# Kernel optimization log

Measured on AMD Instinct MI355X. Metric: run time of the kernel, lower is better.

The kernel has to match this reference:

```python
import jax, jax.numpy as jnp
import numpy as np

# init config (matches init_kwargs)
NO_TRANS = False
SPATIAL_SCALE = 0.0625
POOLED = 7
SAMPLES = 2          # sampling_ratio (sample_per_part)
TRANS_STD = 0.1

B, C, H, W = 2, 256, 96, 96
N_ROIS = 512


def setup_inputs() -> dict:
    key = jax.random.key(0)
    k1, k2, k3, k4, k5 = jax.random.split(key, 5)
    bottom_data = jax.random.normal(k1, (B, C, H, W), dtype=jnp.float32)
    img = H / SPATIAL_SCALE  # image-space extent (1536)
    bidx = jax.random.randint(k2, (N_ROIS,), 0, B).astype(jnp.float32)
    xy1 = jax.random.uniform(k3, (N_ROIS, 2), minval=0.0, maxval=0.7 * img)
    wh = jax.random.uniform(k4, (N_ROIS, 2), minval=0.05 * img, maxval=0.3 * img)
    bottom_rois = jnp.concatenate([bidx[:, None], xy1, xy1 + wh], axis=1)  # [N,5]
    bottom_trans = jax.random.normal(k5, (N_ROIS, 2, POOLED, POOLED), dtype=jnp.float32)
    return {"bottom_data": bottom_data, "bottom_rois": bottom_rois, "bottom_trans": bottom_trans}


def _deform_psroi_pool(feat, rois, trans):
    # feat [B,C,H,W], rois [N,5], trans [N,2,P,P] -> out [N,C,P,P]
    Hf, Wf = feat.shape[2], feat.shape[3]
    b = rois[:, 0].astype(jnp.int32)                                    # [N]
    # CUDA kernel rounds roi coords, shifts by -0.5
    x1 = jnp.round(rois[:, 1]) * SPATIAL_SCALE - 0.5
    y1 = jnp.round(rois[:, 2]) * SPATIAL_SCALE - 0.5
    x2 = (jnp.round(rois[:, 3]) + 1.0) * SPATIAL_SCALE - 0.5
    y2 = (jnp.round(rois[:, 4]) + 1.0) * SPATIAL_SCALE - 0.5
    rw = jnp.maximum(x2 - x1, 0.1)
    rh = jnp.maximum(y2 - y1, 0.1)
    bin_w = rw / POOLED
    bin_h = rh / POOLED
    sub_w = bin_w / SAMPLES
    sub_h = bin_h / SAMPLES

    grid = jnp.arange(POOLED, dtype=feat.dtype)
    # part_size == pooled_size and group_size == 1 -> part_h=ph, part_w=pw, class 0
    if NO_TRANS:
        trans_x = jnp.zeros((rois.shape[0], POOLED, POOLED), feat.dtype)
        trans_y = trans_x
    else:
        trans_x = trans[:, 0] * TRANS_STD  # [N,P,P]
        trans_y = trans[:, 1] * TRANS_STD

    # bin start coords per (n, ph, pw)
    wstart = grid[None, None, :] * bin_w[:, None, None] + x1[:, None, None] + trans_x * rw[:, None, None]
    hstart = grid[None, :, None] * bin_h[:, None, None] + y1[:, None, None] + trans_y * rh[:, None, None]

    s = jnp.arange(SAMPLES, dtype=feat.dtype)
    # sample coords [N,P,P,S(ih),S(iw)]
    w = wstart[:, :, :, None, None] + s[None, None, None, None, :] * sub_w[:, None, None, None, None]
    h = hstart[:, :, :, None, None] + s[None, None, None, :, None] * sub_h[:, None, None, None, None]

    valid = (w >= -0.5) & (w <= Wf - 0.5) & (h >= -0.5) & (h <= Hf - 0.5)
    wc = jnp.clip(w, 0.0, Wf - 1.0)
    hc = jnp.clip(h, 0.0, Hf - 1.0)
    x0 = jnp.floor(wc); y0 = jnp.floor(hc)
    dx = wc - x0; dy = hc - y0
    x0i = x0.astype(jnp.int32); y0i = y0.astype(jnp.int32)
    x1i = jnp.ceil(wc).astype(jnp.int32); y1i = jnp.ceil(hc).astype(jnp.int32)

    feat_hwc = jnp.transpose(feat, (0, 2, 3, 1))  # [B,H,W,C]
    bb = b[:, None, None, None, None]

    def gather(yi, xi):
        return feat_hwc[bb, yi, xi]  # [N,P,P,S,S,C]

    w00 = ((1.0 - dx) * (1.0 - dy))[..., None]
    w01 = (dx * (1.0 - dy))[..., None]
    w10 = ((1.0 - dx) * dy)[..., None]
    w11 = (dx * dy)[..., None]
    val = (w00 * gather(y0i, x0i) + w01 * gather(y0i, x1i)
           + w10 * gather(y1i, x0i) + w11 * gather(y1i, x1i))
    val = jnp.where(valid[..., None], val, 0.0)

    ssum = val.sum(axis=(3, 4))                              # [N,P,P,C]
    count = valid.astype(feat.dtype).sum(axis=(3, 4))        # [N,P,P]
    out = jnp.where(count[..., None] > 0, ssum / jnp.maximum(count[..., None], 1.0), 0.0)
    return jnp.transpose(out, (0, 3, 1, 2))                  # [N,C,P,P]


def reference(bottom_data, bottom_rois, bottom_trans):
    return _deform_psroi_pool(bottom_data, bottom_rois, bottom_trans)
```

## Files before the change

### kernel.cpp

```cpp
#include <hip/hip_runtime.h>

#define B_      2
#define C_      256
#define H_      96
#define W_      96
#define HW_     (H_ * W_)
#define P_      7
#define PP_     (P_ * P_)
#define NROIS_  512
#define SCALE_  0.0625f
#define TSTD_   0.1f

#define NGROUP_ 8
#define GC_     (C_ / NGROUP_)

__device__ __forceinline__ unsigned f2bf(float f) {
    union { float f; unsigned u; } x; x.f = f;
    return (x.u + 0x7fffu + ((x.u >> 16) & 1u)) >> 16;
}
__device__ __forceinline__ float bf_lo(unsigned u) {
    union { unsigned i; float f; } x; x.i = u << 16; return x.f;
}
__device__ __forceinline__ float bf_hi(unsigned u) {
    union { unsigned i; float f; } x; x.i = u & 0xffff0000u; return x.f;
}

__global__ __launch_bounds__(256) void nchw_to_gp_bf16(const float* __restrict__ in,
                                                       ushort* __restrict__ out) {
    __shared__ float tile[32][33];
    const int b   = blockIdx.z;
    const int g   = blockIdx.x & (NGROUP_ - 1);
    const int p0  = (blockIdx.x >> 3) * 32;
    const int c0  = g * 32;
    const int tid = threadIdx.x;

    const float* src = in + (size_t)b * (C_ * HW_);
    ushort*      dst = out + ((size_t)(b * NGROUP_ + g) * HW_) * GC_;

    const int px = tid & 31, cr = tid >> 5;
#pragma unroll
    for (int k = 0; k < 32; k += 8)
        tile[cr + k][px] =
            __builtin_nontemporal_load(&src[(size_t)(c0 + cr + k) * HW_ + p0 + px]);
    __syncthreads();

    const int cp = tid & 15, py = tid >> 4;
    unsigned* dst32 = (unsigned*)dst;
#pragma unroll
    for (int k = 0; k < 32; k += 16) {
        const int p = py + k;
        const unsigned u0 = f2bf(tile[2 * cp + 0][p]);
        const unsigned u1 = f2bf(tile[2 * cp + 1][p]);
        dst32[(size_t)(p0 + p) * (GC_ / 2) + cp] = u0 | (u1 << 16);
    }
}

__global__ __launch_bounds__(256) void dpsroi_pool4(const ushort* __restrict__ feat,
                                                    const float* __restrict__ rois,
                                                    const float* __restrict__ trans,
                                                    float* __restrict__ out) {
    __shared__ float sout[GC_ * PP_];

    const int blk = blockIdx.x;
    const int g   = blk & (NGROUP_ - 1);
    const int n   = blk >> 3;
    const int tid = threadIdx.x;
    const int bin = tid >> 2;
    const int ch0 = (tid & 3) * 8;

    const int   broi = (int)rois[n * 5 + 0];
    const float x1 = rintf(rois[n * 5 + 1]) * SCALE_ - 0.5f;
    const float y1 = rintf(rois[n * 5 + 2]) * SCALE_ - 0.5f;
    const float x2 = (rintf(rois[n * 5 + 3]) + 1.0f) * SCALE_ - 0.5f;
    const float y2 = (rintf(rois[n * 5 + 4]) + 1.0f) * SCALE_ - 0.5f;
    const float rw = fmaxf(x2 - x1, 0.1f);
    const float rh = fmaxf(y2 - y1, 0.1f);
    const float bin_w = rw * (1.0f / 7.0f);
    const float bin_h = rh * (1.0f / 7.0f);
    const float sub_w = bin_w * 0.5f;
    const float sub_h = bin_h * 0.5f;

    const ushort* fb = feat + ((size_t)(broi * NGROUP_ + g) * HW_) * GC_ + ch0;

    float acc[8] = {0.f, 0.f, 0.f, 0.f, 0.f, 0.f, 0.f, 0.f};
    int cnt = 0;

    if (bin < PP_) {
        const int pi = bin / P_;
        const int pj = bin - pi * P_;
        const float tx = trans[((n * 2 + 0) * P_ + pi) * P_ + pj] * TSTD_;
        const float ty = trans[((n * 2 + 1) * P_ + pi) * P_ + pj] * TSTD_;
        const float wstart = (float)pj * bin_w + x1 + tx * rw;
        const float hstart = (float)pi * bin_h + y1 + ty * rh;

        float wt[4][4];
        int   ofs[4][4];
#pragma unroll
        for (int s = 0; s < 4; ++s) {
            const float w = wstart + (float)(s & 1) * sub_w;
            const float h = hstart + (float)(s >> 1) * sub_h;
            const bool valid = (w >= -0.5f) & (w <= (float)W_ - 0.5f) &
                               (h >= -0.5f) & (h <= (float)H_ - 0.5f);
            cnt += valid ? 1 : 0;
            const float vf = valid ? 1.0f : 0.0f;
            const float wc  = fminf(fmaxf(w, 0.0f), (float)(W_ - 1));
            const float hc  = fminf(fmaxf(h, 0.0f), (float)(H_ - 1));
            const float x0f = floorf(wc), y0f = floorf(hc);
            const float dx  = wc - x0f,   dy  = hc - y0f;
            const int   x0  = (int)x0f,   y0  = (int)y0f;
            const int   xp  = (int)ceilf(wc), yp = (int)ceilf(hc);
            wt[s][0] = vf * (1.0f - dx) * (1.0f - dy);
            wt[s][1] = vf * dx * (1.0f - dy);
            wt[s][2] = vf * (1.0f - dx) * dy;
            wt[s][3] = vf * dx * dy;
            ofs[s][0] = y0 * W_ + x0;
            ofs[s][1] = y0 * W_ + xp;
            ofs[s][2] = yp * W_ + x0;
            ofs[s][3] = yp * W_ + xp;
        }

#pragma unroll
        for (int s = 0; s < 4; ++s) {
            uint4 v[4];
#pragma unroll
            for (int c = 0; c < 4; ++c)
                v[c] = *(const uint4*)(fb + (size_t)ofs[s][c] * GC_);
#pragma unroll
            for (int c = 0; c < 4; ++c) {
                const float wgt = wt[s][c];
                acc[0] += wgt * bf_lo(v[c].x);
                acc[1] += wgt * bf_hi(v[c].x);
                acc[2] += wgt * bf_lo(v[c].y);
                acc[3] += wgt * bf_hi(v[c].y);
                acc[4] += wgt * bf_lo(v[c].z);
                acc[5] += wgt * bf_hi(v[c].z);
                acc[6] += wgt * bf_lo(v[c].w);
                acc[7] += wgt * bf_hi(v[c].w);
            }
        }

        const float inv = (cnt > 0) ? (1.0f / (float)cnt) : 0.0f;
#pragma unroll
        for (int j = 0; j < 8; ++j)
            sout[(ch0 + j) * PP_ + bin] = acc[j] * inv;
    }

    __syncthreads();
    float* outn = out + ((size_t)n * C_ + g * GC_) * PP_;
    for (int f = tid; f < GC_ * PP_; f += 256)
        __builtin_nontemporal_store(sout[f], &outn[f]);
}

extern "C" void kernel_launch(void* const* d_in, const int* in_sizes, int n_in,
                              void* d_out, int out_size, void* d_ws, size_t ws_size,
                              hipStream_t stream) {
    const float* feat  = (const float*)d_in[0];
    const float* rois  = (const float*)d_in[1];
    const float* trans = (const float*)d_in[2];
    float* out = (float*)d_out;

    ushort* gp = (ushort*)d_ws;
    dim3 tb(256);
    dim3 tg((HW_ / 32) * NGROUP_, 1, B_);
    nchw_to_gp_bf16<<<tg, tb, 0, stream>>>(feat, gp);
    dpsroi_pool4<<<NROIS_ * NGROUP_, 256, 0, stream>>>(gp, rois, trans, out);
}
```

Measured before the change: 92.54 us.

## Assign channel groups to blocks by XCC id through per-group atomic work queues

Each block reads its hardware XCC id and takes a (roi, channel-group) work item from a per-group atomic counter, so every XCC mostly handles a single channel group. The aim is to keep each group's bf16 feature slice resident in that XCC's own L2 instead of spreading all groups across every XCC. A counter-zeroing kernel launch, one atomic per block and a block-wide sync are added, and work is taken from neighbouring groups when a queue runs dry. It depends on the XCC_ID hardware register encoding and on the workspace being larger than 32 MB.

```diff
diff --git a/kernel.cpp b/kernel.cpp
--- a/kernel.cpp
+++ b/kernel.cpp
@@ -14,6 +14,8 @@
 #define NGROUP_ 8
 #define GC_     (C_ / NGROUP_)
 
+#define XCC_ID_IMM 6164
+
 __device__ __forceinline__ unsigned f2bf(float f) {
     union { float f; unsigned u; } x; x.f = f;
     return (x.u + 0x7fffu + ((x.u >> 16) & 1u)) >> 16;
@@ -23,6 +25,10 @@
 }
 __device__ __forceinline__ float bf_hi(unsigned u) {
     union { unsigned i; float f; } x; x.i = u & 0xffff0000u; return x.f;
+}
+
+__global__ void zero_counters(int* __restrict__ c) {
+    if (threadIdx.x < NGROUP_) c[threadIdx.x] = 0;
 }
 
 __global__ __launch_bounds__(256) void nchw_to_gp_bf16(const float* __restrict__ in,
@@ -55,16 +61,33 @@
     }
 }
 
-__global__ __launch_bounds__(256) void dpsroi_pool4(const ushort* __restrict__ feat,
+__global__ __launch_bounds__(256) void dpsroi_pool5(const ushort* __restrict__ feat,
                                                     const float* __restrict__ rois,
                                                     const float* __restrict__ trans,
-                                                    float* __restrict__ out) {
+                                                    float* __restrict__ out,
+                                                    int* __restrict__ qcnt) {
     __shared__ float sout[GC_ * PP_];
+    __shared__ int   s_item;
 
-    const int blk = blockIdx.x;
-    const int g   = blk & (NGROUP_ - 1);
-    const int n   = blk >> 3;
     const int tid = threadIdx.x;
+
+    if (tid == 0) {
+        const int xcc = __builtin_amdgcn_s_getreg(XCC_ID_IMM) & (NGROUP_ - 1);
+        int item = -1;
+#pragma unroll 1
+        for (int t = 0; t < NGROUP_ && item < 0; ++t) {
+            const int gg  = (xcc + t) & (NGROUP_ - 1);
+            const int idx = atomicAdd(&qcnt[gg], 1);
+            if (idx < NROIS_) item = (idx << 3) | gg;
+        }
+        s_item = item;
+    }
+    __syncthreads();
+    const int item = s_item;
+    if (item < 0) return;
+    const int g = item & (NGROUP_ - 1);
+    const int n = item >> 3;
+
     const int bin = tid >> 2;
     const int ch0 = (tid & 3) * 8;
 
@@ -82,9 +105,6 @@
 
     const ushort* fb = feat + ((size_t)(broi * NGROUP_ + g) * HW_) * GC_ + ch0;
 
-    float acc[8] = {0.f, 0.f, 0.f, 0.f, 0.f, 0.f, 0.f, 0.f};
-    int cnt = 0;
-
     if (bin < PP_) {
         const int pi = bin / P_;
         const int pj = bin - pi * P_;
@@ -95,6 +115,7 @@
 
         float wt[4][4];
         int   ofs[4][4];
+        int   cnt = 0;
 #pragma unroll
         for (int s = 0; s < 4; ++s) {
             const float w = wstart + (float)(s & 1) * sub_w;
@@ -119,6 +140,7 @@
             ofs[s][3] = yp * W_ + xp;
         }
 
+        float acc[8] = {0.f, 0.f, 0.f, 0.f, 0.f, 0.f, 0.f, 0.f};
 #pragma unroll
         for (int s = 0; s < 4; ++s) {
             uint4 v[4];
@@ -159,9 +181,12 @@
     const float* trans = (const float*)d_in[2];
     float* out = (float*)d_out;
 
-    ushort* gp = (ushort*)d_ws;
+    ushort* gp  = (ushort*)d_ws;
+    int*    qct = (int*)((char*)d_ws + (32u << 20));
+
+    zero_counters<<<1, 64, 0, stream>>>(qct);
     dim3 tb(256);
     dim3 tg((HW_ / 32) * NGROUP_, 1, B_);
     nchw_to_gp_bf16<<<tg, tb, 0, stream>>>(feat, gp);
-    dpsroi_pool4<<<NROIS_ * NGROUP_, 256, 0, stream>>>(gp, rois, trans, out);
+    dpsroi_pool5<<<NROIS_ * NGROUP_, 256, 0, stream>>>(gp, rois, trans, out, qct);
 }
```

Result: slower. 128.4 us (+38.7%).
